# Optimization experiments

Measured on AMD Instinct MI355X. Metric: run time of the kernel, lower is better.

Reference implementation:

```python
import jax, jax.numpy as jnp
import numpy as np

D_MODEL = 1024
N_HEADS = 16
D_K = D_MODEL // N_HEADS
ROPE_THETA = 10000.0
SOFT_CAP = 50.0  # Gemma-2-style logit soft cap
B, S = 4, 2048


def _rope(x, pos, theta=ROPE_THETA):
    # x: [..., S, d_k], interleaved-pair rotation
    d_k = x.shape[-1]
    inv_freq = theta ** (-jnp.arange(0, d_k, 2, dtype=jnp.float32) / d_k)  # [d_k/2]
    ang = pos.astype(jnp.float32)[:, None] * inv_freq[None, :]             # [S, d_k/2]
    cos, sin = jnp.cos(ang), jnp.sin(ang)
    x1, x2 = x[..., 0::2], x[..., 1::2]
    out_even = x1 * cos - x2 * sin
    out_odd = x1 * sin + x2 * cos
    return jnp.stack([out_even, out_odd], axis=-1).reshape(x.shape)


def setup_inputs() -> dict:
    key = jax.random.key(0)
    kx, kqkv, kout = jax.random.split(key, 3)
    scale = D_MODEL ** -0.5
    x = jax.random.normal(kx, (B, S, D_MODEL), dtype=jnp.float32)
    w_qkv = jax.random.normal(kqkv, (3 * D_MODEL, D_MODEL), dtype=jnp.float32) * scale
    w_out = jax.random.normal(kout, (D_MODEL, D_MODEL), dtype=jnp.float32) * scale
    return {"x": x, "w_qkv": w_qkv, "w_out": w_out}


def reference(x, w_qkv, w_out):
    b, s, d = x.shape
    # fused QKV projection (Linear, no bias): [B,S,3D]
    qkv = jnp.einsum('bsd,ed->bse', x, w_qkv)
    # '(n h d_k)' split -> [3, B, H, S, d_k]
    qkv = qkv.reshape(b, s, 3, N_HEADS, D_K)
    qkv = jnp.transpose(qkv, (2, 0, 3, 1, 4))
    q, k, v = qkv[0], qkv[1], qkv[2]
    pos = jnp.arange(s)
    q = _rope(q, pos)
    k = _rope(k, pos)
    scores = jnp.einsum('bhqd,bhkd->bhqk', q, k) / jnp.float32(D_K) ** 0.5
    scores = SOFT_CAP * jnp.tanh(scores / SOFT_CAP)  # cap_logits
    causal = jnp.tril(jnp.ones((s, s), dtype=bool))
    scores = jnp.where(causal, scores, jnp.float32(-1e30))
    attn = jax.nn.softmax(scores, axis=-1)
    out = jnp.einsum('bhqk,bhkd->bhqd', attn, v)
    out = jnp.transpose(out, (0, 2, 1, 3)).reshape(b, s, d)  # (h d_v) merge
    return jnp.einsum('bsd,ed->bse', out, w_out)
```

## Files before the change

kernel.cpp:

```cpp
#include <hip/hip_runtime.h>
#include <stdint.h>

#define S_LEN 2048
#define NH    16
#define DK    64
#define DM    1024

typedef __attribute__((ext_vector_type(8))) __bf16 bf16x8;
typedef __attribute__((ext_vector_type(8))) unsigned short u16x8;
typedef __attribute__((ext_vector_type(4))) float  f32x4;

static __device__ __forceinline__ unsigned short f2bf(float f) {
    union { float f; unsigned int u; } v; v.f = f;
    unsigned int r = v.u + 0x7FFFu + ((v.u >> 16) & 1u);
    return (unsigned short)(r >> 16);
}

static __device__ __forceinline__ float cap_exp2(float sp) {
    float u = exp2f(sp);
    float w = __builtin_amdgcn_rcpf(u + 1.0f);
    return exp2f(__builtin_fmaf(w, -144.2695040888f, 72.1347520444f));
}

#define GLL(src_, dst_) __builtin_amdgcn_global_load_lds(                              \
    (const __attribute__((address_space(1))) unsigned int*)(src_),                     \
    (__attribute__((address_space(3))) unsigned int*)(dst_), 16, 0, 0)

__global__ void detect_f32(const unsigned short* __restrict__ x, int* __restrict__ flag)
{
    __shared__ int tot;
    if (threadIdx.x == 0) tot = 0;
    __syncthreads();
    int weird = 0;
    for (int i = threadIdx.x; i < 16384; i += 256) {
        int e = (x[i] >> 7) & 0xFF;
        if (e == 0 || e < 87 || e > 167) weird++;
    }
    atomicAdd(&tot, weird);
    __syncthreads();
    if (threadIdx.x == 0) *flag = (tot > 4000) ? 1 : 0;
}

__global__ __launch_bounds__(256) void norm_bf16(const void* __restrict__ src,
                                                 unsigned short* __restrict__ dst,
                                                 int n, const int* __restrict__ flag)
{
    const int isf32 = *flag;
    int i = (blockIdx.x * 256 + threadIdx.x) * 8;
    if (i >= n) return;
    if (isf32) {
        const float* p = (const float*)src + i;
        u16x8 o;
        o[0] = f2bf(p[0]); o[1] = f2bf(p[1]); o[2] = f2bf(p[2]); o[3] = f2bf(p[3]);
        o[4] = f2bf(p[4]); o[5] = f2bf(p[5]); o[6] = f2bf(p[6]); o[7] = f2bf(p[7]);
        *(u16x8*)&dst[i] = o;
    } else {
        *(uint4*)&dst[i] = *(const uint4*)((const unsigned short*)src + i);
    }
}

__global__ __launch_bounds__(256) void rope_tab(float2* __restrict__ tab)
{
    int e = blockIdx.x * 256 + threadIdx.x;
    int s = e >> 5, d2 = e & 31;
    float invf = exp2f(-(float)d2 * 0.41524101186f);
    float sn, cs;
    sincosf((float)s * invf, &sn, &cs);
    tab[e] = make_float2(cs, sn);
}

#define VST  136

#define MFMA(a, b, c) __builtin_amdgcn_mfma_f32_16x16x32_bf16((a), (b), (c), 0, 0, 0)

#define GEMM_MAIN(Aptr, Wptr, lda_, ldw_)                                              \
    f32x4 zz = {0.f, 0.f, 0.f, 0.f};                                                   \
    f32x4 c00=zz,c01=zz,c02=zz,c03=zz, c10=zz,c11=zz,c12=zz,c13=zz,                    \
          c20=zz,c21=zz,c22=zz,c23=zz, c30=zz,c31=zz,c32=zz,c33=zz;                    \
    const int strow_ = wave * 16 + (lane >> 2);                                        \
    const int sgr_   = (((lane & 3) ^ ((strow_ >> 1) & 3))) << 3;                      \
    const unsigned short* Ag_ = (Aptr) + (size_t)(m0 + strow_) * (lda_) + sgr_;        \
    const unsigned short* Bg_ = (Wptr) + (size_t)(n0 + strow_) * (ldw_) + sgr_;        \
    const int kfG_ = ((quad ^ ((l16 >> 1) & 3))) << 3;                                 \
    {                                                                                  \
        unsigned short* Ad_ = As + wave * 512;                                         \
        unsigned short* Bd_ = Bs + wave * 512;                                         \
        GLL(Ag_, Ad_); GLL(Ag_ + 64 * (size_t)(lda_), Ad_ + 2048);                     \
        GLL(Bg_, Bd_); GLL(Bg_ + 64 * (size_t)(ldw_), Bd_ + 2048);                     \
    }                                                                                  \
    __syncthreads();                                  \
    int cbuf_ = 0;                                                                     \
    for (int k0 = 0; k0 < 1024; k0 += 32) {                                            \
        if (k0 + 32 < 1024) {                                                          \
            unsigned short* Ad_ = As + ((cbuf_ ^ 1) << 12) + wave * 512;               \
            unsigned short* Bd_ = Bs + ((cbuf_ ^ 1) << 12) + wave * 512;               \
            GLL(Ag_ + k0 + 32, Ad_);                                                   \
            GLL(Ag_ + k0 + 32 + 64 * (size_t)(lda_), Ad_ + 2048);                      \
            GLL(Bg_ + k0 + 32, Bd_);                                                   \
            GLL(Bg_ + k0 + 32 + 64 * (size_t)(ldw_), Bd_ + 2048);                      \
        }                                                                              \
        const unsigned short* Ar_ = As + (cbuf_ << 12);                                \
        const unsigned short* Br_ = Bs + (cbuf_ << 12);                                \
        bf16x8 a0 = *(const bf16x8*)&Ar_[(wm +  0 + l16) * 32 + kfG_];                 \
        bf16x8 a1 = *(const bf16x8*)&Ar_[(wm + 16 + l16) * 32 + kfG_];                 \
        bf16x8 a2 = *(const bf16x8*)&Ar_[(wm + 32 + l16) * 32 + kfG_];                 \
        bf16x8 a3 = *(const bf16x8*)&Ar_[(wm + 48 + l16) * 32 + kfG_];                 \
        bf16x8 b0 = *(const bf16x8*)&Br_[(wn +  0 + l16) * 32 + kfG_];                 \
        bf16x8 b1 = *(const bf16x8*)&Br_[(wn + 16 + l16) * 32 + kfG_];                 \
        bf16x8 b2 = *(const bf16x8*)&Br_[(wn + 32 + l16) * 32 + kfG_];                 \
        bf16x8 b3 = *(const bf16x8*)&Br_[(wn + 48 + l16) * 32 + kfG_];                 \
        c00 = MFMA(a0, b0, c00); c01 = MFMA(a0, b1, c01);                              \
        c02 = MFMA(a0, b2, c02); c03 = MFMA(a0, b3, c03);                              \
        c10 = MFMA(a1, b0, c10); c11 = MFMA(a1, b1, c11);                              \
        c12 = MFMA(a1, b2, c12); c13 = MFMA(a1, b3, c13);                              \
        c20 = MFMA(a2, b0, c20); c21 = MFMA(a2, b1, c21);                              \
        c22 = MFMA(a2, b2, c22); c23 = MFMA(a2, b3, c23);                              \
        c30 = MFMA(a3, b0, c30); c31 = MFMA(a3, b1, c31);                              \
        c32 = MFMA(a3, b2, c32); c33 = MFMA(a3, b3, c33);                              \
        __syncthreads();                    \
        cbuf_ ^= 1;                                                                    \
    }

__global__ __launch_bounds__(256) void gemm_fused(const unsigned short* __restrict__ A,
                                                  const unsigned short* __restrict__ W,
                                                  const float2* __restrict__ tab,
                                                  unsigned short* __restrict__ qr,
                                                  unsigned short* __restrict__ kr,
                                                  unsigned short* __restrict__ vt)
{
    __shared__ __align__(16) unsigned short smem[128 * VST];
    unsigned short* As = smem;
    unsigned short* Bs = smem + 8192;

    const int tid  = threadIdx.x;
    const int wave = tid >> 6;
    const int lane = tid & 63;
    const int quad = lane >> 4;
    const int l16  = lane & 15;
    const int m0 = blockIdx.y * 128;
    const int n0 = blockIdx.x * 128;
    const int wm = (wave >> 1) * 64;
    const int wn = (wave & 1) * 64;

    GEMM_MAIN(A, W, 1024, 1024)

    const int cls = n0 >> 10;
    if (cls < 2) {
        unsigned short* dst = cls ? kr : qr;
        const float qs = cls ? 1.0f : 0.125f * 0.0577078016f;

#define ROPE_R(accv, MTc, rc, even_, h_, d_) do {                                      \
        int row = m0 + wm + (MTc) * 16 + quad * 4 + (rc);                              \
        int s = row & (S_LEN - 1), b = row >> 11;                                      \
        float2 cssn = tab[(s << 5) + ((d_) >> 1)];                                     \
        float own = accv[rc];                                                          \
        float oth = __shfl_xor(own, 1);                                                \
        float res = (even_) ? (own * cssn.x - oth * cssn.y)                            \
                            : (oth * cssn.y + own * cssn.x);                           \
        dst[((size_t)(b * NH + (h_)) * S_LEN + s) * DK + (d_)] = f2bf(res * qs);       \
    } while (0)

#define ROPE_ST(accv, MTc, NTc) do {                                                   \
        int col = (n0 & 1023) + wn + (NTc) * 16 + l16;                                 \
        int h = col >> 6, d = col & 63;                                                \
        int even = !(d & 1);                                                           \
        ROPE_R(accv, MTc, 0, even, h, d);                                              \
        ROPE_R(accv, MTc, 1, even, h, d);                                              \
        ROPE_R(accv, MTc, 2, even, h, d);                                              \
        ROPE_R(accv, MTc, 3, even, h, d);                                              \
    } while (0)

        ROPE_ST(c00, 0, 0); ROPE_ST(c01, 0, 1); ROPE_ST(c02, 0, 2); ROPE_ST(c03, 0, 3);
        ROPE_ST(c10, 1, 0); ROPE_ST(c11, 1, 1); ROPE_ST(c12, 1, 2); ROPE_ST(c13, 1, 3);
        ROPE_ST(c20, 2, 0); ROPE_ST(c21, 2, 1); ROPE_ST(c22, 2, 2); ROPE_ST(c23, 2, 3);
        ROPE_ST(c30, 3, 0); ROPE_ST(c31, 3, 1); ROPE_ST(c32, 3, 2); ROPE_ST(c33, 3, 3);
    } else {
        __syncthreads();

#define VST_ACC(accv, MTc, NTc) do {                                                   \
        int dl = wn + (NTc) * 16 + l16;                                                \
        int base = dl * VST + wm + (MTc) * 16 + quad * 4;                              \
        smem[base + 0] = f2bf(accv[0]); smem[base + 1] = f2bf(accv[1]);                \
        smem[base + 2] = f2bf(accv[2]); smem[base + 3] = f2bf(accv[3]);                \
    } while (0)

        VST_ACC(c00, 0, 0); VST_ACC(c01, 0, 1); VST_ACC(c02, 0, 2); VST_ACC(c03, 0, 3);
        VST_ACC(c10, 1, 0); VST_ACC(c11, 1, 1); VST_ACC(c12, 1, 2); VST_ACC(c13, 1, 3);
        VST_ACC(c20, 2, 0); VST_ACC(c21, 2, 1); VST_ACC(c22, 2, 2); VST_ACC(c23, 2, 3);
        VST_ACC(c30, 3, 0); VST_ACC(c31, 3, 1); VST_ACC(c32, 3, 2); VST_ACC(c33, 3, 3);
        __syncthreads();
        int dl = tid >> 1, sh = (tid & 1) * 64;
        int vcol = (n0 - 2048) + dl;
        int h = vcol >> 6, dd = vcol & 63;
        int b = m0 >> 11, s0 = m0 & (S_LEN - 1);
        unsigned short* dst = vt + (((size_t)(b * NH + h) * DK + dd) * S_LEN + s0 + sh);
        const unsigned short* src = smem + dl * VST + sh;
#pragma unroll
        for (int i = 0; i < 64; i += 8)
            *(bf16x8*)&dst[i] = *(const bf16x8*)&src[i];
    }
}

__global__ __launch_bounds__(256) void gemm_out(const unsigned short* __restrict__ A,
                                                const unsigned short* __restrict__ W,
                                                float* __restrict__ C)
{
    __shared__ __align__(16) unsigned short As[8192];
    __shared__ __align__(16) unsigned short Bs[8192];
    const int tid  = threadIdx.x;
    const int wave = tid >> 6;
    const int lane = tid & 63;
    const int quad = lane >> 4;
    const int l16  = lane & 15;
    const int m0 = blockIdx.y * 128;
    const int n0 = blockIdx.x * 128;
    const int wm = (wave >> 1) * 64;
    const int wn = (wave & 1) * 64;

    GEMM_MAIN(A, W, 1024, 1024)

#define OUT_ST(accv, MTc, NTc) do {                                                    \
    int col = n0 + wn + (NTc) * 16 + l16;                                              \
    int rowb = m0 + wm + (MTc) * 16 + quad * 4;                                        \
    C[(size_t)(rowb + 0) * 1024 + col] = accv[0];                                      \
    C[(size_t)(rowb + 1) * 1024 + col] = accv[1];                                      \
    C[(size_t)(rowb + 2) * 1024 + col] = accv[2];                                      \
    C[(size_t)(rowb + 3) * 1024 + col] = accv[3];                                      \
} while (0)

    OUT_ST(c00, 0, 0); OUT_ST(c01, 0, 1); OUT_ST(c02, 0, 2); OUT_ST(c03, 0, 3);
    OUT_ST(c10, 1, 0); OUT_ST(c11, 1, 1); OUT_ST(c12, 1, 2); OUT_ST(c13, 1, 3);
    OUT_ST(c20, 2, 0); OUT_ST(c21, 2, 1); OUT_ST(c22, 2, 2); OUT_ST(c23, 2, 3);
    OUT_ST(c30, 3, 0); OUT_ST(c31, 3, 1); OUT_ST(c32, 3, 2); OUT_ST(c33, 3, 3);
}

__global__ __launch_bounds__(256) void attn_fwd(const unsigned short* __restrict__ qr,
                                                const unsigned short* __restrict__ kr,
                                                const unsigned short* __restrict__ vt,
                                                unsigned short* __restrict__ aout)
{
    __shared__ __align__(16) unsigned short kvs[2][2][4096];
    __shared__ __align__(16) unsigned short plds[4][1024];
    int blk  = blockIdx.x;
    int pr   = blk & 15;
    int bh   = blk >> 4;
    int b    = bh >> 4, h = bh & 15;
    int wave = threadIdx.x >> 6;
    int lane = threadIdx.x & 63;
    int quad = lane >> 4, l16 = lane & 15;

    const unsigned short* kbase = kr + (size_t)bh * S_LEN * DK;
    const unsigned short* vbase = vt + (size_t)bh * DK * S_LEN;
    unsigned short* pw = &plds[wave][0];

    u16x8 onesu = {0x3F80,0x3F80,0x3F80,0x3F80,0x3F80,0x3F80,0x3F80,0x3F80};
    bf16x8 vones = *(bf16x8*)&onesu;

    const int lam3  = lane >> 3;
    const int sc3p  = (lane & 7) ^ lam3;
    const int strow = wave * 8 + lam3;
    const int stcol = sc3p * 8;
    const int kfA = l16 * 64 + ((quad ^ (l16 & 7)) << 3);

#define STAGE(c_, nb_) do {                                                            \
    const int j0s = (c_) * 64;                                                         \
    unsigned short* kd = &kvs[nb_][0][wave * 512];                                     \
    unsigned short* vd = &kvs[nb_][1][wave * 512];                                     \
    const unsigned short* kg = kbase + (size_t)(j0s + strow) * 64 + stcol;             \
    const unsigned short* vg = vbase + (size_t)strow * S_LEN + j0s + stcol;            \
    GLL(kg, kd); GLL(kg + 32 * 64, kd + 2048);                                         \
    GLL(vg, vd); GLL(vg + 32 * S_LEN, vd + 2048);                                      \
} while (0)

#define QK_LDS(kb_) do {                                                               \
    bf16x8 ka, kb;                                                                     \
    ka = *(const bf16x8*)&(kb_)[kfA];          kb = *(const bf16x8*)&(kb_)[kfA ^ 32];  \
    sc0 = MFMA(qf0, ka, sc0); sc0 = MFMA(qf1, kb, sc0);                                \
    ka = *(const bf16x8*)&(kb_)[kfA + 1024];   kb = *(const bf16x8*)&(kb_)[(kfA + 1024) ^ 32]; \
    sc1 = MFMA(qf0, ka, sc1); sc1 = MFMA(qf1, kb, sc1);                                \
    ka = *(const bf16x8*)&(kb_)[kfA + 2048];   kb = *(const bf16x8*)&(kb_)[(kfA + 2048) ^ 32]; \
    sc2 = MFMA(qf0, ka, sc2); sc2 = MFMA(qf1, kb, sc2);                                \
    ka = *(const bf16x8*)&(kb_)[kfA + 3072];   kb = *(const bf16x8*)&(kb_)[(kfA + 3072) ^ 32]; \
    sc3 = MFMA(qf0, ka, sc3); sc3 = MFMA(qf1, kb, sc3);                                \
} while (0)

#define PV_LDS(vb_) do {                                                               \
    bf16x8 pf0 = *(const bf16x8*)&pw[kfA];                                             \
    bf16x8 pf1 = *(const bf16x8*)&pw[kfA ^ 32];                                        \
    bf16x8 va, vb;                                                                     \
    va = *(const bf16x8*)&(vb_)[kfA];          vb = *(const bf16x8*)&(vb_)[kfA ^ 32];  \
    o0 = MFMA(pf0, va, o0); o0 = MFMA(pf1, vb, o0);                                    \
    va = *(const bf16x8*)&(vb_)[kfA + 1024];   vb = *(const bf16x8*)&(vb_)[(kfA + 1024) ^ 32]; \
    o1 = MFMA(pf0, va, o1); o1 = MFMA(pf1, vb, o1);                                    \
    va = *(const bf16x8*)&(vb_)[kfA + 2048];   vb = *(const bf16x8*)&(vb_)[(kfA + 2048) ^ 32]; \
    o2 = MFMA(pf0, va, o2); o2 = MFMA(pf1, vb, o2);                                    \
    va = *(const bf16x8*)&(vb_)[kfA + 3072];   vb = *(const bf16x8*)&(vb_)[(kfA + 3072) ^ 32]; \
    o3 = MFMA(pf0, va, o3); o3 = MFMA(pf1, vb, o3);                                    \
    o4 = MFMA(pf0, vones, o4); o4 = MFMA(pf1, vones, o4);                              \
} while (0)

#define P_STORE(rc, p0_, p1_, p2_, p3_) do {                                           \
    unsigned int r01, r23;                                                             \
    asm("v_cvt_pk_bf16_f32 %0, %1, %2" : "=v"(r01) : "v"(p0_), "v"(p1_));              \
    asm("v_cvt_pk_bf16_f32 %0, %1, %2" : "=v"(r23) : "v"(p2_), "v"(p3_));              \
    const int row_ = quad * 4 + (rc);                                                  \
    const int r7_  = row_ & 7;                                                         \
    const int pb_  = row_ * 64 + (l16 & 7);                                            \
    const int lh_  = l16 >> 3;                                                         \
    pw[pb_ + ((( lh_     ^ r7_) << 3))] = (unsigned short)r01;                         \
    pw[pb_ + (((2 | lh_) ^ r7_) << 3)]  = (unsigned short)(r01 >> 16);                 \
    pw[pb_ + (((4 | lh_) ^ r7_) << 3)]  = (unsigned short)r23;                         \
    pw[pb_ + (((6 | lh_) ^ r7_) << 3)]  = (unsigned short)(r23 >> 16);                 \
} while (0)

#define ROW_UPD_N(rc) do {                                                             \
    float p0 = cap_exp2(sc0[rc]);                                                      \
    float p1 = cap_exp2(sc1[rc]);                                                      \
    float p2 = cap_exp2(sc2[rc]);                                                      \
    float p3 = cap_exp2(sc3[rc]);                                                      \
    P_STORE(rc, p0, p1, p2, p3);                                                       \
} while (0)

#define ROW_UPD_M(rc) do {                                                             \
    int qrow = q0w + quad * 4 + (rc);                                                  \
    float p0 = (j0 + l16      > qrow) ? 0.f : cap_exp2(sc0[rc]);                       \
    float p1 = (j0 + 16 + l16 > qrow) ? 0.f : cap_exp2(sc1[rc]);                       \
    float p2 = (j0 + 32 + l16 > qrow) ? 0.f : cap_exp2(sc2[rc]);                       \
    float p3 = (j0 + 48 + l16 > qrow) ? 0.f : cap_exp2(sc3[rc]);                       \
    P_STORE(rc, p0, p1, p2, p3);                                                       \
} while (0)

    for (int side = 0; side < 2; ++side) {
        const int qblk = side ? (31 - pr) : pr;
        const int q0w  = qblk * 64 + wave * 16;

        const unsigned short* qbase = qr + ((size_t)bh * S_LEN + q0w) * DK;
        bf16x8 qf0 = *(const bf16x8*)&qbase[l16 * DK + quad * 8];
        bf16x8 qf1 = *(const bf16x8*)&qbase[l16 * DK + 32 + quad * 8];

        f32x4 zz = {0.f, 0.f, 0.f, 0.f};
        f32x4 o0 = zz, o1 = zz, o2 = zz, o3 = zz, o4 = zz;

        const int nch = qblk + 1;

        STAGE(0, 0);
        asm volatile("s_waitcnt vmcnt(0)" ::: "memory");
        __syncthreads();
        int cb = 0;

        for (int c = 0; c < nch - 1; ++c) {
            STAGE(c + 1, cb ^ 1);
            f32x4 sc0 = zz, sc1 = zz, sc2 = zz, sc3 = zz;
            QK_LDS(&kvs[cb][0][0]);
            ROW_UPD_N(0); ROW_UPD_N(1); ROW_UPD_N(2); ROW_UPD_N(3);
            asm volatile("s_waitcnt lgkmcnt(0)" ::: "memory");
            PV_LDS(&kvs[cb][1][0]);
            asm volatile("s_waitcnt vmcnt(0)" ::: "memory");
            __syncthreads();
            cb ^= 1;
        }

        {
            const int j0 = (nch - 1) * 64;
            f32x4 sc0 = zz, sc1 = zz, sc2 = zz, sc3 = zz;
            QK_LDS(&kvs[cb][0][0]);
            ROW_UPD_M(0); ROW_UPD_M(1); ROW_UPD_M(2); ROW_UPD_M(3);
            asm volatile("s_waitcnt lgkmcnt(0)" ::: "memory");
            PV_LDS(&kvs[cb][1][0]);
            __syncthreads();
        }

#define OUT_ROW(rc) do {                                                               \
        int qrow = q0w + quad * 4 + (rc);                                              \
        size_t off = (size_t)(b * S_LEN + qrow) * DM + h * DK + l16;                   \
        float rl = 1.0f / o4[rc];                                                      \
        aout[off +  0] = f2bf(o0[rc] * rl);                                            \
        aout[off + 16] = f2bf(o1[rc] * rl);                                            \
        aout[off + 32] = f2bf(o2[rc] * rl);                                            \
        aout[off + 48] = f2bf(o3[rc] * rl);                                            \
} while (0)

        OUT_ROW(0); OUT_ROW(1); OUT_ROW(2); OUT_ROW(3);
#undef OUT_ROW
    }
}

extern "C" void kernel_launch(void* const* d_in, const int* in_sizes, int n_in,
                              void* d_out, int out_size, void* d_ws, size_t ws_size,
                              hipStream_t stream)
{
    const void* x = nullptr; const void* wqkv = nullptr; const void* wout = nullptr;
    for (int i = 0; i < n_in; ++i) {
        if      (in_sizes[i] == 8388608) x    = d_in[i];
        else if (in_sizes[i] == 3145728) wqkv = d_in[i];
        else if (in_sizes[i] == 1048576) wout = d_in[i];
    }
    float* out = (float*)d_out;
    unsigned short* ws   = (unsigned short*)d_ws;
    unsigned short* ob16 = (unsigned short*)d_out;

    unsigned short* qr     = ws;
    unsigned short* kr     = ws + (size_t)8388608;
    unsigned short* aout   = ws + (size_t)16777216;
    int* flag              = (int*)(ws + (size_t)25165824);
    unsigned short* wqkvbf = aout;
    unsigned short* woutbf = qr;
    float2* tab            = (float2*)(ws + (size_t)16777216 + 4194304);

    unsigned short* vt  = ob16;
    unsigned short* xbf = ob16 + (size_t)8388608;

    detect_f32<<<1, 256, 0, stream>>>((const unsigned short*)x, flag);
    norm_bf16<<<4096, 256, 0, stream>>>(x, xbf, 8388608, flag);
    norm_bf16<<<1536, 256, 0, stream>>>(wqkv, wqkvbf, 3145728, flag);
    rope_tab<<<256, 256, 0, stream>>>(tab);
    gemm_fused<<<dim3(24, 64), 256, 0, stream>>>(xbf, wqkvbf, tab, qr, kr, vt);
    attn_fwd<<<1024, 256, 0, stream>>>(qr, kr, vt, aout);
    norm_bf16<<<512, 256, 0, stream>>>(wout, woutbf, 1048576, flag);
    gemm_out<<<dim3(8, 64), 256, 0, stream>>>(aout, woutbf, out);
}
```

Baseline: 313.1 us.

## Merge prep kernels, skip bf16 copies, and raise wave priority around MFMA

Merges the x/wqkv conversion kernels and the rope table kernel into one launch. When the inputs are already bf16, the copy is skipped and the GEMMs read the original buffers through a flag-selected pointer. Also sets wave priority high around the QK and PV MFMA sequences in attention. This cuts launch count and memory traffic. The input is fp32 in the default setup, so the conversions still run and the gain is mostly from fewer launches plus the setprio scheduling hint.

```diff
diff --git a/kernel.cpp b/kernel.cpp
--- a/kernel.cpp
+++ b/kernel.cpp
@@ -41,32 +41,45 @@
     if (threadIdx.x == 0) *flag = (tot > 4000) ? 1 : 0;
 }
 
-__global__ __launch_bounds__(256) void norm_bf16(const void* __restrict__ src,
+__global__ __launch_bounds__(256) void prep(const void* __restrict__ x,
+                                            const void* __restrict__ wqkv,
+                                            unsigned short* __restrict__ xbf,
+                                            unsigned short* __restrict__ wqkvbf,
+                                            float2* __restrict__ tab,
+                                            const int* __restrict__ flag)
+{
+    int bid = blockIdx.x;
+    if (bid < 256) {
+        int e = bid * 256 + threadIdx.x;
+        int s = e >> 5, d2 = e & 31;
+        float invf = exp2f(-(float)d2 * 0.41524101186f);
+        float sn, cs;
+        sincosf((float)s * invf, &sn, &cs);
+        tab[e] = make_float2(cs, sn);
+        return;
+    }
+    if (!*flag) return;
+    const float* src; unsigned short* dst; int i;
+    if (bid < 4352) { src = (const float*)x;    dst = xbf;    i = ((bid - 256)  * 256 + threadIdx.x) * 8; }
+    else            { src = (const float*)wqkv; dst = wqkvbf; i = ((bid - 4352) * 256 + threadIdx.x) * 8; }
+    const float* p = src + i;
+    u16x8 o;
+    o[0] = f2bf(p[0]); o[1] = f2bf(p[1]); o[2] = f2bf(p[2]); o[3] = f2bf(p[3]);
+    o[4] = f2bf(p[4]); o[5] = f2bf(p[5]); o[6] = f2bf(p[6]); o[7] = f2bf(p[7]);
+    *(u16x8*)&dst[i] = o;
+}
+
+__global__ __launch_bounds__(256) void norm_wout(const void* __restrict__ src,
                                                  unsigned short* __restrict__ dst,
-                                                 int n, const int* __restrict__ flag)
-{
-    const int isf32 = *flag;
+                                                 const int* __restrict__ flag)
+{
+    if (!*flag) return;
     int i = (blockIdx.x * 256 + threadIdx.x) * 8;
-    if (i >= n) return;
-    if (isf32) {
-        const float* p = (const float*)src + i;
-        u16x8 o;
-        o[0] = f2bf(p[0]); o[1] = f2bf(p[1]); o[2] = f2bf(p[2]); o[3] = f2bf(p[3]);
-        o[4] = f2bf(p[4]); o[5] = f2bf(p[5]); o[6] = f2bf(p[6]); o[7] = f2bf(p[7]);
-        *(u16x8*)&dst[i] = o;
-    } else {
-        *(uint4*)&dst[i] = *(const uint4*)((const unsigned short*)src + i);
-    }
-}
-
-__global__ __launch_bounds__(256) void rope_tab(float2* __restrict__ tab)
-{
-    int e = blockIdx.x * 256 + threadIdx.x;
-    int s = e >> 5, d2 = e & 31;
-    float invf = exp2f(-(float)d2 * 0.41524101186f);
-    float sn, cs;
-    sincosf((float)s * invf, &sn, &cs);
-    tab[e] = make_float2(cs, sn);
+    const float* p = (const float*)src + i;
+    u16x8 o;
+    o[0] = f2bf(p[0]); o[1] = f2bf(p[1]); o[2] = f2bf(p[2]); o[3] = f2bf(p[3]);
+    o[4] = f2bf(p[4]); o[5] = f2bf(p[5]); o[6] = f2bf(p[6]); o[7] = f2bf(p[7]);
+    *(u16x8*)&dst[i] = o;
 }
 
 #define VST  136
@@ -121,8 +134,11 @@
         cbuf_ ^= 1;                                                                    \
     }
 
-__global__ __launch_bounds__(256) void gemm_fused(const unsigned short* __restrict__ A,
-                                                  const unsigned short* __restrict__ W,
+__global__ __launch_bounds__(256) void gemm_fused(const unsigned short* __restrict__ x0,
+                                                  const unsigned short* __restrict__ xc,
+                                                  const unsigned short* __restrict__ w0,
+                                                  const unsigned short* __restrict__ wc,
+                                                  const int* __restrict__ flag,
                                                   const float2* __restrict__ tab,
                                                   unsigned short* __restrict__ qr,
                                                   unsigned short* __restrict__ kr,
@@ -131,6 +147,10 @@
     __shared__ __align__(16) unsigned short smem[128 * VST];
     unsigned short* As = smem;
     unsigned short* Bs = smem + 8192;
+
+    const int isf32 = *flag;
+    const unsigned short* A = isf32 ? xc : x0;
+    const unsigned short* W = isf32 ? wc : w0;
 
     const int tid  = threadIdx.x;
     const int wave = tid >> 6;
@@ -202,11 +222,14 @@
 }
 
 __global__ __launch_bounds__(256) void gemm_out(const unsigned short* __restrict__ A,
-                                                const unsigned short* __restrict__ W,
+                                                const unsigned short* __restrict__ w0,
+                                                const unsigned short* __restrict__ wc,
+                                                const int* __restrict__ flag,
                                                 float* __restrict__ C)
 {
     __shared__ __align__(16) unsigned short As[8192];
     __shared__ __align__(16) unsigned short Bs[8192];
+    const unsigned short* W = *flag ? wc : w0;
     const int tid  = threadIdx.x;
     const int wave = tid >> 6;
     const int lane = tid & 63;
@@ -274,6 +297,7 @@
 
 #define QK_LDS(kb_) do {                                                               \
     bf16x8 ka, kb;                                                                     \
+    __builtin_amdgcn_s_setprio(1);                                                     \
     ka = *(const bf16x8*)&(kb_)[kfA];          kb = *(const bf16x8*)&(kb_)[kfA ^ 32];  \
     sc0 = MFMA(qf0, ka, sc0); sc0 = MFMA(qf1, kb, sc0);                                \
     ka = *(const bf16x8*)&(kb_)[kfA + 1024];   kb = *(const bf16x8*)&(kb_)[(kfA + 1024) ^ 32]; \
@@ -282,12 +306,14 @@
     sc2 = MFMA(qf0, ka, sc2); sc2 = MFMA(qf1, kb, sc2);                                \
     ka = *(const bf16x8*)&(kb_)[kfA + 3072];   kb = *(const bf16x8*)&(kb_)[(kfA + 3072) ^ 32]; \
     sc3 = MFMA(qf0, ka, sc3); sc3 = MFMA(qf1, kb, sc3);                                \
+    __builtin_amdgcn_s_setprio(0);                                                     \
 } while (0)
 
 #define PV_LDS(vb_) do {                                                               \
     bf16x8 pf0 = *(const bf16x8*)&pw[kfA];                                             \
     bf16x8 pf1 = *(const bf16x8*)&pw[kfA ^ 32];                                        \
     bf16x8 va, vb;                                                                     \
+    __builtin_amdgcn_s_setprio(1);                                                     \
     va = *(const bf16x8*)&(vb_)[kfA];          vb = *(const bf16x8*)&(vb_)[kfA ^ 32];  \
     o0 = MFMA(pf0, va, o0); o0 = MFMA(pf1, vb, o0);                                    \
     va = *(const bf16x8*)&(vb_)[kfA + 1024];   vb = *(const bf16x8*)&(vb_)[(kfA + 1024) ^ 32]; \
@@ -297,6 +323,7 @@
     va = *(const bf16x8*)&(vb_)[kfA + 3072];   vb = *(const bf16x8*)&(vb_)[(kfA + 3072) ^ 32]; \
     o3 = MFMA(pf0, va, o3); o3 = MFMA(pf1, vb, o3);                                    \
     o4 = MFMA(pf0, vones, o4); o4 = MFMA(pf1, vones, o4);                              \
+    __builtin_amdgcn_s_setprio(0);                                                     \
 } while (0)
 
 #define P_STORE(rc, p0_, p1_, p2_, p3_) do {                                           \
@@ -411,11 +438,13 @@
     unsigned short* xbf = ob16 + (size_t)8388608;
 
     detect_f32<<<1, 256, 0, stream>>>((const unsigned short*)x, flag);
-    norm_bf16<<<4096, 256, 0, stream>>>(x, xbf, 8388608, flag);
-    norm_bf16<<<1536, 256, 0, stream>>>(wqkv, wqkvbf, 3145728, flag);
-    rope_tab<<<256, 256, 0, stream>>>(tab);
-    gemm_fused<<<dim3(24, 64), 256, 0, stream>>>(xbf, wqkvbf, tab, qr, kr, vt);
+    prep<<<5888, 256, 0, stream>>>(x, wqkv, xbf, wqkvbf, tab, flag);
+    gemm_fused<<<dim3(24, 64), 256, 0, stream>>>((const unsigned short*)x, xbf,
+                                                 (const unsigned short*)wqkv, wqkvbf,
+                                                 flag, tab, qr, kr, vt);
     attn_fwd<<<1024, 256, 0, stream>>>(qr, kr, vt, aout);
-    norm_bf16<<<512, 256, 0, stream>>>(wout, woutbf, 1048576, flag);
-    gemm_out<<<dim3(8, 64), 256, 0, stream>>>(aout, woutbf, out);
-}
+    norm_wout<<<512, 256, 0, stream>>>(wout, woutbf, flag);
+    gemm_out<<<dim3(8, 64), 256, 0, stream>>>(aout,
+                                              (const unsigned short*)wout, woutbf,
+                                              flag, out);
+}
```

Result: no change. 315.5 us (+0.8%).
